# Optimization experiments

Measured on AMD Instinct MI355X. Metric: run time of the kernel, lower is better.

## Reference

```python
import jax, jax.numpy as jnp
import numpy as np

N_NODES = 100000
N_EDGES = 1600000
NODE_DIM = 128
EDGE_DIM = 64
MSG_DIM = 128
NODE_DIM_OUT = 128


def setup_inputs() -> dict:
    key = jax.random.key(0)
    k1, k2, k3, k4, k5, k6, k7 = jax.random.split(key, 7)
    node_emb = jax.random.normal(k1, (N_NODES, NODE_DIM), dtype=jnp.float32)
    edge_index = jax.random.randint(k2, (2, N_EDGES), 0, N_NODES, dtype=jnp.int64)
    edge_emb = jax.random.normal(k3, (N_EDGES, EDGE_DIM), dtype=jnp.float32)
    # Linear params (stored as [in, out]; torch uses [out, in] with x @ W.T)
    s_msg = 1.0 / np.sqrt(NODE_DIM + EDGE_DIM)
    W_msg = jax.random.uniform(k4, (NODE_DIM + EDGE_DIM, MSG_DIM), jnp.float32, -s_msg, s_msg)
    b_msg = jax.random.uniform(k5, (MSG_DIM,), jnp.float32, -s_msg, s_msg)
    s_upd = 1.0 / np.sqrt(NODE_DIM + MSG_DIM)
    W_upd = jax.random.uniform(k6, (NODE_DIM + MSG_DIM, NODE_DIM_OUT), jnp.float32, -s_upd, s_upd)
    b_upd = jax.random.uniform(k7, (NODE_DIM_OUT,), jnp.float32, -s_upd, s_upd)
    return {"node_emb": node_emb, "edge_index": edge_index, "edge_emb": edge_emb,
            "W_msg": W_msg, "b_msg": b_msg, "W_upd": W_upd, "b_upd": b_upd}


def reference(node_emb, edge_index, edge_emb, W_msg, b_msg, W_upd, b_upd):
    # PyG MessagePassing default flow: x_j = x[edge_index[0]] (source),
    # messages aggregated (mean) at edge_index[1] (target).
    src = edge_index[0]
    dst = edge_index[1]
    n = node_emb.shape[0]

    x_j = node_emb[src]                                    # [E, node_dim] gather
    msg_in = jnp.concatenate([x_j, edge_emb], axis=1)      # [E, node_dim+edge_dim]
    msg = jax.nn.relu(msg_in @ W_msg + b_msg)              # [E, msg_dim]

    # scatter-mean aggregate to nodes
    summed = jax.ops.segment_sum(msg, dst, num_segments=n)  # [N, msg_dim]
    counts = jax.ops.segment_sum(jnp.ones((msg.shape[0],), dtype=msg.dtype), dst, num_segments=n)
    mean_msg = summed / jnp.maximum(counts, 1.0)[:, None]

    upd_in = jnp.concatenate([node_emb, mean_msg], axis=1)  # [N, node_dim+msg_dim]
    h = jax.nn.relu(upd_in @ W_upd + b_upd)                 # [N, node_dim_out]
    # dropout is identity in eval mode; normalize=False (default)
    return h
```

## Files before the change

### kernel.cpp

```cpp
#include <hip/hip_runtime.h>
#include <hip/hip_bf16.h>

#define N_NODES 100000
#define N_EDGES 1600000
#define D_NODE 128
#define D_EDGE 64
#define D_MSG 128
#define K1 192
#define K2 256
#define D_OUT 128
#define NSB 98
#define TILE 64
#define NT (N_EDGES / TILE)

using frag8 = __attribute__((ext_vector_type(8))) short;
using facc  = __attribute__((ext_vector_type(4))) float;

static __device__ __forceinline__ unsigned short f2bf(float f) {
    unsigned int u = __float_as_uint(f);
    u = u + 0x7fffu + ((u >> 16) & 1u);
    return (unsigned short)(u >> 16);
}
static __device__ __forceinline__ float bflo(unsigned int u) { return __uint_as_float(u << 16); }
static __device__ __forceinline__ float bfhi(unsigned int u) { return __uint_as_float(u & 0xffff0000u); }

union F8 { unsigned short s[8]; frag8 f; uint4 u4; };

static __device__ __forceinline__ frag8 pack8(float4 a, float4 b) {
    F8 u;
    u.s[0] = f2bf(a.x); u.s[1] = f2bf(a.y); u.s[2] = f2bf(a.z); u.s[3] = f2bf(a.w);
    u.s[4] = f2bf(b.x); u.s[5] = f2bf(b.y); u.s[6] = f2bf(b.z); u.s[7] = f2bf(b.w);
    return u.f;
}

__global__ void prep_all_kernel(const float* __restrict__ Wm, const float* __restrict__ Wu,
                                const float* __restrict__ node_emb, const int* __restrict__ dst,
                                unsigned short* __restrict__ WtM, unsigned short* __restrict__ WtU,
                                unsigned int* __restrict__ nodeB32, int* __restrict__ cnt) {
    int idx0 = blockIdx.x * blockDim.x + threadIdx.x;
    int stride = gridDim.x * blockDim.x;
    for (int idx = idx0; idx < 128 * K1; idx += stride) {
        int o = idx / K1, k = idx - o * K1;
        WtM[idx] = f2bf(Wm[k * D_MSG + o]);
    }
    for (int idx = idx0; idx < 128 * K2; idx += stride) {
        int o = idx >> 8, k = idx & 255;
        WtU[idx] = f2bf(Wu[k * D_OUT + o]);
    }
    const int total = N_NODES * 64;
    for (int i = idx0; i < total; i += stride) {
        float2 v = *(const float2*)&node_emb[(size_t)i * 2];
        nodeB32[i] = (unsigned)f2bf(v.x) | ((unsigned)f2bf(v.y) << 16);
    }
    for (int e = idx0; e < N_EDGES; e += stride) {
        int d = min(max(dst[e], 0), N_NODES - 1);
        atomicAdd(&cnt[d], 1);
    }
}

__global__ __launch_bounds__(1024) void scan_blocks(const int* __restrict__ cnt,
                                                    int* __restrict__ base,
                                                    int* __restrict__ part) {
    __shared__ int sh[1024];
    int i = blockIdx.x * 1024 + threadIdx.x;
    int c = (i < N_NODES) ? cnt[i] : 0;
    sh[threadIdx.x] = c;
    __syncthreads();
    for (int s = 1; s < 1024; s <<= 1) {
        int t = (threadIdx.x >= s) ? sh[threadIdx.x - s] : 0;
        __syncthreads();
        sh[threadIdx.x] += t;
        __syncthreads();
    }
    if (i < N_NODES) base[i] = sh[threadIdx.x] - c;
    if (threadIdx.x == 1023) part[blockIdx.x] = sh[1023];
}

__global__ __launch_bounds__(128) void scan_partials(int* __restrict__ part) {
    __shared__ int sh[128];
    int i = threadIdx.x;
    int c = (i < NSB) ? part[i] : 0;
    sh[i] = c;
    __syncthreads();
    for (int s = 1; s < 128; s <<= 1) {
        int t = (i >= s) ? sh[i - s] : 0;
        __syncthreads();
        sh[i] += t;
        __syncthreads();
    }
    if (i < NSB) part[i] = sh[i] - c;
}

__global__ __launch_bounds__(1024) void scan_add(int* __restrict__ base, const int* __restrict__ part) {
    int i = blockIdx.x * 1024 + threadIdx.x;
    if (i < N_NODES) base[i] += part[blockIdx.x];
}

__global__ void scatter_kernel(const int* __restrict__ dst, const int* __restrict__ src,
                               const int* __restrict__ base, int* __restrict__ cursor,
                               int* __restrict__ perm, int* __restrict__ srcS,
                               int* __restrict__ dstS) {
    int idx0 = blockIdx.x * blockDim.x + threadIdx.x;
    int stride = gridDim.x * blockDim.x;
    for (int e = idx0; e < N_EDGES; e += stride) {
        int d = min(max(dst[e], 0), N_NODES - 1);
        int pos = base[d] + atomicAdd(&cursor[d], 1);
        perm[pos] = e;
        srcS[pos] = src[e];
        dstS[pos] = d;
    }
}

__global__ __launch_bounds__(256, 4) void msg_fused_kernel(
    const unsigned short* __restrict__ nodeB, const int* __restrict__ srcS,
    const int* __restrict__ perm, const int* __restrict__ dstS,
    const float* __restrict__ edge_emb, const unsigned short* __restrict__ WtM,
    const float* __restrict__ b_msg, const int* __restrict__ base,
    const int* __restrict__ cnt, unsigned int* __restrict__ meanB32,
    float* __restrict__ spill)
{
    __shared__ unsigned short sIn[TILE][192];
    __shared__ unsigned short sMsg[TILE][128];

    const int lane = threadIdx.x & 63;
    const int wav  = threadIdx.x >> 6;
    const int j = lane & 15;
    const int q = lane >> 4;

    frag8 wfr[2][6];
#pragma unroll
    for (int m2 = 0; m2 < 2; ++m2) {
        const unsigned short* wrow = WtM + ((wav * 2 + m2) * 16 + j) * K1;
#pragma unroll
        for (int kc = 0; kc < 6; ++kc)
            wfr[m2][kc] = *(const frag8*)&wrow[(kc * 4 + q) * 8];
    }
    float bias[2][4];
#pragma unroll
    for (int m2 = 0; m2 < 2; ++m2)
#pragma unroll
        for (int r = 0; r < 4; ++r) bias[m2][r] = b_msg[(wav * 2 + m2) * 16 + q * 4 + r];

    const int eL = threadIdx.x >> 2;
    const int qt = threadIdx.x & 3;
    const int swz = eL & 7;

    uint4  nst[4];
    float4 est[4];

    const int t0 = blockIdx.x;

    {
        const int e = t0 * TILE + eL;
        const int sp = min(max(srcS[e], 0), N_NODES - 1);
        const unsigned short* nrow = nodeB + (size_t)sp * D_NODE + qt * 32;
#pragma unroll
        for (int i = 0; i < 4; ++i) nst[i] = *(const uint4*)&nrow[i * 8];
        const float* erow = edge_emb + (size_t)perm[e] * D_EDGE + qt * 16;
#pragma unroll
        for (int i = 0; i < 4; ++i) est[i] = *(const float4*)&erow[i * 4];
    }

#pragma unroll 1
    for (int t = t0; t < NT; t += gridDim.x) {
        const int e0 = t * TILE;

        __syncthreads();

        {
            unsigned short* drow = &sIn[eL][0];
#pragma unroll
            for (int i = 0; i < 4; ++i)
                *(uint4*)&drow[((4 * qt + i) ^ swz) * 8] = nst[i];
#pragma unroll
            for (int h = 0; h < 2; ++h) {
                F8 u;
                u.f = pack8(est[h * 2], est[h * 2 + 1]);
                *(uint4*)&drow[((16 + 2 * qt + h) ^ swz) * 8] = u.u4;
            }
        }
        __syncthreads();

        const int tn = t + gridDim.x;
        if (tn < NT) {
            const int e = tn * TILE + eL;
            const int sp = min(max(srcS[e], 0), N_NODES - 1);
            const unsigned short* nrow = nodeB + (size_t)sp * D_NODE + qt * 32;
#pragma unroll
            for (int i = 0; i < 4; ++i) nst[i] = *(const uint4*)&nrow[i * 8];
            const float* erow = edge_emb + (size_t)perm[e] * D_EDGE + qt * 16;
#pragma unroll
            for (int i = 0; i < 4; ++i) est[i] = *(const float4*)&erow[i * 4];
        }

        facc acc[2][4];
#pragma unroll
        for (int m2 = 0; m2 < 2; ++m2)
#pragma unroll
            for (int eg = 0; eg < 4; ++eg) { facc z = {0.f,0.f,0.f,0.f}; acc[m2][eg] = z; }

        const int rsw = j & 7;
#pragma unroll
        for (int eg = 0; eg < 4; ++eg) {
            const unsigned short* irow = &sIn[eg * 16 + j][0];
#pragma unroll
            for (int kc = 0; kc < 6; ++kc) {
                frag8 b = *(const frag8*)&irow[((4 * kc + q) ^ rsw) * 8];
                acc[0][eg] = __builtin_amdgcn_mfma_f32_16x16x32_bf16(wfr[0][kc], b, acc[0][eg], 0, 0, 0);
                acc[1][eg] = __builtin_amdgcn_mfma_f32_16x16x32_bf16(wfr[1][kc], b, acc[1][eg], 0, 0, 0);
            }
        }

#pragma unroll
        for (int eg = 0; eg < 4; ++eg) {
            unsigned short* mrow = &sMsg[eg * 16 + j][0];
#pragma unroll
            for (int m2 = 0; m2 < 2; ++m2) {
                float v0 = fmaxf(acc[m2][eg][0] + bias[m2][0], 0.f);
                float v1 = fmaxf(acc[m2][eg][1] + bias[m2][1], 0.f);
                float v2 = fmaxf(acc[m2][eg][2] + bias[m2][2], 0.f);
                float v3 = fmaxf(acc[m2][eg][3] + bias[m2][3], 0.f);
                uint2 w;
                w.x = (unsigned)f2bf(v0) | ((unsigned)f2bf(v1) << 16);
                w.y = (unsigned)f2bf(v2) | ((unsigned)f2bf(v3) << 16);
                int c64 = wav * 8 + m2 * 4 + q;
                *(uint2*)&mrow[(c64 ^ rsw) * 4] = w;
            }
        }
        __syncthreads();

        const int d_lo = dstS[e0];
        const int d_hi = dstS[e0 + TILE - 1];
        for (int n = d_lo + wav; n <= d_hi; n += 4) {
            const int b = base[n];
            const int c = cnt[n];
            const int lo = max(b - e0, 0);
            const int hi = min(b + c - e0, TILE);
            float s0 = 0.f, s1 = 0.f;
            for (int r = lo; r < hi; ++r) {
                const unsigned* mr = (const unsigned*)&sMsg[r][0];
                unsigned u = mr[(((lane >> 1) ^ (r & 7)) << 1) | (lane & 1)];
                s0 += bflo(u); s1 += bfhi(u);
            }
            const float inv = 1.0f / fmaxf((float)c, 1.0f);
            s0 *= inv; s1 *= inv;
            if (b >= e0 && b + c <= e0 + TILE) {
                meanB32[(size_t)n * 64 + lane] =
                    (unsigned)f2bf(s0) | ((unsigned)f2bf(s1) << 16);
            } else {
                int slot = (n == d_lo) ? 0 : 1;
                *(float2*)(spill + ((size_t)(t * 2 + slot)) * D_MSG + lane * 2) =
                    make_float2(s0, s1);
            }
        }
    }
}

__global__ __launch_bounds__(256) void cleanup_kernel(
    const int* __restrict__ dstS, const int* __restrict__ base,
    const int* __restrict__ cnt, const float* __restrict__ spill,
    unsigned int* __restrict__ meanB32)
{
    const int wav = threadIdx.x >> 6;
    const int lane = threadIdx.x & 63;
    const int n = blockIdx.x * 4 + wav;
    const int c = cnt[n];
    float s0 = 0.f, s1 = 0.f;
    if (c > 0) {
        const int b = base[n];
        const int t0 = b >> 6, t1 = (b + c - 1) >> 6;
        if (t0 == t1) return;
        for (int t = t0; t <= t1; ++t) {
            const int slot = (dstS[t * TILE] == n) ? 0 : 1;
            const float* sp = spill + ((size_t)(t * 2 + slot)) * D_MSG + lane * 2;
            s0 += sp[0]; s1 += sp[1];
        }
    }
    meanB32[(size_t)n * 64 + lane] = (unsigned)f2bf(s0) | ((unsigned)f2bf(s1) << 16);
}

__global__ __launch_bounds__(256) void node_gemm_kernel(
    const unsigned short* __restrict__ nodeB, const unsigned short* __restrict__ meanB,
    const unsigned short* __restrict__ WtU, const float* __restrict__ b_upd,
    float* __restrict__ out)
{
    __shared__ unsigned short sW[128 * K2];

    for (int idx = threadIdx.x; idx < 128 * 32; idx += 256) {
        int o = idx >> 5, ch = idx & 31;
        *(uint4*)&sW[o * K2 + (ch ^ (o & 7)) * 8] = *(const uint4*)&WtU[o * K2 + ch * 8];
    }

    const int lane = threadIdx.x & 63;
    const int wav  = threadIdx.x >> 6;
    const int j = lane & 15;
    const int q = lane >> 4;
    const int rs = j & 7;

    float bias[32];
#pragma unroll
    for (int mt = 0; mt < 8; ++mt)
#pragma unroll
        for (int r = 0; r < 4; ++r) bias[mt * 4 + r] = b_upd[mt * 16 + q * 4 + r];
    __syncthreads();

    const int n0w = blockIdx.x * 256 + wav * 64;

#pragma unroll 1
    for (int g = 0; g < 4; ++g) {
        const int n = n0w + g * 16 + j;
        const bool valid = (n < N_NODES);
        const size_t nn = valid ? (size_t)n : 0;

        frag8 bfr[8];
        const unsigned short* nrow = nodeB + nn * D_NODE;
#pragma unroll
        for (int kc = 0; kc < 4; ++kc)
            bfr[kc] = *(const frag8*)&nrow[kc * 32 + q * 8];
        const unsigned short* mrow = meanB + nn * D_MSG;
#pragma unroll
        for (int kc = 0; kc < 4; ++kc)
            bfr[4 + kc] = *(const frag8*)&mrow[kc * 32 + q * 8];

        facc acc[8];
#pragma unroll
        for (int mt = 0; mt < 8; ++mt) { facc z = {0.f, 0.f, 0.f, 0.f}; acc[mt] = z; }

#pragma unroll
        for (int mt = 0; mt < 8; ++mt) {
            const unsigned short* wrow = &sW[(mt * 16 + j) * K2];
#pragma unroll
            for (int kc = 0; kc < 8; ++kc) {
                frag8 a = *(const frag8*)&wrow[((kc * 4 + q) ^ rs) * 8];
                acc[mt] = __builtin_amdgcn_mfma_f32_16x16x32_bf16(a, bfr[kc], acc[mt], 0, 0, 0);
            }
        }

        if (valid) {
            float* orow = out + (size_t)n * D_OUT;
#pragma unroll
            for (int mt = 0; mt < 8; ++mt)
#pragma unroll
                for (int r = 0; r < 4; ++r)
                    orow[mt * 16 + q * 4 + r] = fmaxf(acc[mt][r] + bias[mt * 4 + r], 0.f);
        }
    }
}

__global__ void prep_w_kernel(const float* __restrict__ Wm, const float* __restrict__ Wu,
                              unsigned short* __restrict__ WtM, unsigned short* __restrict__ WtU) {
    int idx0 = blockIdx.x * blockDim.x + threadIdx.x;
    int stride = gridDim.x * blockDim.x;
    for (int idx = idx0; idx < 128 * K1; idx += stride) {
        int o = idx / K1, k = idx - o * K1;
        WtM[idx] = f2bf(Wm[k * D_MSG + o]);
    }
    for (int idx = idx0; idx < 128 * K2; idx += stride) {
        int o = idx >> 8, k = idx & 255;
        WtU[idx] = f2bf(Wu[k * D_OUT + o]);
    }
}

__global__ void hist_kernel(const int* __restrict__ dst, int* __restrict__ cnt) {
    int idx0 = blockIdx.x * blockDim.x + threadIdx.x;
    int stride = gridDim.x * blockDim.x;
    for (int e = idx0; e < N_EDGES; e += stride) {
        int d = min(max(dst[e], 0), N_NODES - 1);
        atomicAdd(&cnt[d], 1);
    }
}

__global__ __launch_bounds__(256) void msg_agg_kernel_fb(
    const float* __restrict__ node_emb, const int* __restrict__ src,
    const float* __restrict__ edge_emb, const unsigned short* __restrict__ WtM,
    const float* __restrict__ b_msg, const int* __restrict__ perm,
    const int* __restrict__ dstS, const int* __restrict__ cnt,
    float* __restrict__ mean)
{
    __shared__ unsigned short sW[128 * K1];

    for (int idx = threadIdx.x; idx < 128 * 24; idx += 256) {
        int o = idx / 24, ch = idx % 24;
        *(uint4*)&sW[o * K1 + (ch ^ (o & 7)) * 8] = *(const uint4*)&WtM[o * K1 + ch * 8];
    }

    const int lane = threadIdx.x & 63;
    const int wav  = threadIdx.x >> 6;
    const int j = lane & 15;
    const int q = lane >> 4;

    float bias[32];
#pragma unroll
    for (int mt = 0; mt < 8; ++mt)
#pragma unroll
        for (int r = 0; r < 4; ++r) bias[mt * 4 + r] = b_msg[mt * 16 + q * 4 + r];
    __syncthreads();

    const int e0w = blockIdx.x * 256 + wav * 64;
    float carry[32];
    int carry_d = -1;

#pragma unroll 1
    for (int g = 0; g < 4; ++g) {
        const int e = e0w + g * 16 + j;
        const int p = perm[e];
        const int d = dstS[e];
        const int sp = min(max(src[p], 0), N_NODES - 1);
        const float invc = 1.0f / (float)cnt[d];

        frag8 bfr[6];
        const float* nrow = node_emb + (size_t)sp * D_NODE;
#pragma unroll
        for (int kc = 0; kc < 4; ++kc) {
            float4 a = *(const float4*)&nrow[kc * 32 + q * 8];
            float4 c = *(const float4*)&nrow[kc * 32 + q * 8 + 4];
            bfr[kc] = pack8(a, c);
        }
        const float* erow = edge_emb + (size_t)p * D_EDGE;
#pragma unroll
        for (int kc = 0; kc < 2; ++kc) {
            float4 a = *(const float4*)&erow[kc * 32 + q * 8];
            float4 c = *(const float4*)&erow[kc * 32 + q * 8 + 4];
            bfr[4 + kc] = pack8(a, c);
        }

        facc acc[8];
#pragma unroll
        for (int mt = 0; mt < 8; ++mt) { facc z = {0.f, 0.f, 0.f, 0.f}; acc[mt] = z; }

#pragma unroll
        for (int mt = 0; mt < 8; ++mt) {
            const unsigned short* wrow = &sW[(mt * 16 + j) * K1];
            const int rs = j & 7;
#pragma unroll
            for (int kc = 0; kc < 6; ++kc) {
                frag8 a = *(const frag8*)&wrow[((kc * 4 + q) ^ rs) * 8];
                acc[mt] = __builtin_amdgcn_mfma_f32_16x16x32_bf16(a, bfr[kc], acc[mt], 0, 0, 0);
            }
        }

        float v[32];
#pragma unroll
        for (int mt = 0; mt < 8; ++mt)
#pragma unroll
            for (int r = 0; r < 4; ++r) {
                float t = acc[mt][r] + bias[mt * 4 + r];
                v[mt * 4 + r] = fmaxf(t, 0.f) * invc;
            }

        int dprev = __shfl_up(d, 1, 16);
        int head = (j == 0 || d != dprev) ? 1 : 0;
        int seg = head;
#pragma unroll
        for (int s = 1; s < 16; s <<= 1) { int t = __shfl_up(seg, s, 16); if (j >= s) seg += t; }
        int sg1 = __shfl_up(seg, 1, 16);
        int sg2 = __shfl_up(seg, 2, 16);
        int sg4 = __shfl_up(seg, 4, 16);
        int sg8 = __shfl_up(seg, 8, 16);
        bool ok1 = (j >= 1) && (sg1 == seg);
        bool ok2 = (j >= 2) && (sg2 == seg);
        bool ok4 = (j >= 4) && (sg4 == seg);
        bool ok8 = (j >= 8) && (sg8 == seg);

#pragma unroll
        for (int i = 0; i < 32; ++i) { float t = __shfl_up(v[i], 1, 16); if (ok1) v[i] += t; }
#pragma unroll
        for (int i = 0; i < 32; ++i) { float t = __shfl_up(v[i], 2, 16); if (ok2) v[i] += t; }
#pragma unroll
        for (int i = 0; i < 32; ++i) { float t = __shfl_up(v[i], 4, 16); if (ok4) v[i] += t; }
#pragma unroll
        for (int i = 0; i < 32; ++i) { float t = __shfl_up(v[i], 8, 16); if (ok8) v[i] += t; }

        int d0 = __shfl(d, 0, 16);
        if (g > 0) {
            if (d0 != carry_d) {
                if (j == 0) {
                    float* mrow = mean + (size_t)carry_d * D_MSG;
#pragma unroll
                    for (int mt = 0; mt < 8; ++mt)
#pragma unroll
                        for (int r = 0; r < 4; ++r)
                            atomicAdd(&mrow[mt * 16 + q * 4 + r], carry[mt * 4 + r]);
                }
            } else if (seg == 1) {
#pragma unroll
                for (int i = 0; i < 32; ++i) v[i] += carry[i];
            }
        }

#pragma unroll
        for (int i = 0; i < 32; ++i) carry[i] = __shfl(v[i], 15, 16);
        carry_d = __shfl(d, 15, 16);

        int dnext = __shfl_down(d, 1, 16);
        bool tail = (j < 15) ? (dnext != d) : (g == 3);
        if (tail) {
            float* mrow = mean + (size_t)d * D_MSG;
#pragma unroll
            for (int mt = 0; mt < 8; ++mt)
#pragma unroll
                for (int r = 0; r < 4; ++r)
                    atomicAdd(&mrow[mt * 16 + q * 4 + r], v[mt * 4 + r]);
        }
    }
}

__global__ __launch_bounds__(256) void node_kernel_fb(
    const float* __restrict__ node_emb, const float* __restrict__ mean,
    const unsigned short* __restrict__ WtU, const float* __restrict__ b_upd,
    float* __restrict__ out)
{
    __shared__ unsigned short sW[128 * K2];

    for (int idx = threadIdx.x; idx < 128 * 32; idx += 256) {
        int o = idx >> 5, ch = idx & 31;
        *(uint4*)&sW[o * K2 + (ch ^ (o & 7)) * 8] = *(const uint4*)&WtU[o * K2 + ch * 8];
    }

    const int lane = threadIdx.x & 63;
    const int wav  = threadIdx.x >> 6;
    const int j = lane & 15;
    const int q = lane >> 4;

    float bias[32];
#pragma unroll
    for (int mt = 0; mt < 8; ++mt)
#pragma unroll
        for (int r = 0; r < 4; ++r) bias[mt * 4 + r] = b_upd[mt * 16 + q * 4 + r];
    __syncthreads();

    const int n0w = blockIdx.x * 256 + wav * 64;

#pragma unroll 1
    for (int g = 0; g < 4; ++g) {
        const int n = n0w + g * 16 + j;
        const bool valid = (n < N_NODES);
        const size_t nn = valid ? (size_t)n : 0;

        frag8 bfr[8];
        const float* nrow = node_emb + nn * D_NODE;
#pragma unroll
        for (int kc = 0; kc < 4; ++kc) {
            float4 a = *(const float4*)&nrow[kc * 32 + q * 8];
            float4 c = *(const float4*)&nrow[kc * 32 + q * 8 + 4];
            bfr[kc] = pack8(a, c);
        }
        const float* mrow = mean + nn * D_MSG;
#pragma unroll
        for (int kc = 0; kc < 4; ++kc) {
            float4 a = *(const float4*)&mrow[kc * 32 + q * 8];
            float4 c = *(const float4*)&mrow[kc * 32 + q * 8 + 4];
            bfr[4 + kc] = pack8(a, c);
        }

        facc acc[8];
#pragma unroll
        for (int mt = 0; mt < 8; ++mt) { facc z = {0.f, 0.f, 0.f, 0.f}; acc[mt] = z; }

#pragma unroll
        for (int mt = 0; mt < 8; ++mt) {
            const unsigned short* wrow = &sW[(mt * 16 + j) * K2];
            const int rs = j & 7;
#pragma unroll
            for (int kc = 0; kc < 8; ++kc) {
                frag8 a = *(const frag8*)&wrow[((kc * 4 + q) ^ rs) * 8];
                acc[mt] = __builtin_amdgcn_mfma_f32_16x16x32_bf16(a, bfr[kc], acc[mt], 0, 0, 0);
            }
        }

        if (valid) {
            float* orow = out + (size_t)n * D_OUT;
#pragma unroll
            for (int mt = 0; mt < 8; ++mt)
#pragma unroll
                for (int r = 0; r < 4; ++r)
                    orow[mt * 16 + q * 4 + r] = fmaxf(acc[mt][r] + bias[mt * 4 + r], 0.f);
        }
    }
}

extern "C" void kernel_launch(void* const* d_in, const int* in_sizes, int n_in,
                              void* d_out, int out_size, void* d_ws, size_t ws_size,
                              hipStream_t stream) {
    const float* node_emb = (const float*)d_in[0];
    const int*   edge_idx = (const int*)d_in[1];
    const float* edge_emb = (const float*)d_in[2];
    const float* W_msg    = (const float*)d_in[3];
    const float* b_msg    = (const float*)d_in[4];
    const float* W_upd    = (const float*)d_in[5];
    const float* b_upd    = (const float*)d_in[6];
    float* out = (float*)d_out;

    const int* src = edge_idx;
    const int* dst = edge_idx + N_EDGES;

    char* W = (char*)d_ws;

    if (ws_size >= 98000000ULL) {
        unsigned short* meanB = (unsigned short*)(W + 0);
        int* cnt     = (int*)(W + 25600000);
        int* cursor  = (int*)(W + 26000000);
        int* base    = (int*)(W + 26400000);
        int* part    = (int*)(W + 26800000);
        int* perm    = (int*)(W + 26800512);
        int* srcS    = (int*)(W + 33200512);
        int* dstS    = (int*)(W + 39600512);
        unsigned short* WtM   = (unsigned short*)(W + 46000512);
        unsigned short* WtU   = (unsigned short*)(W + 46049664);
        unsigned short* nodeB = (unsigned short*)(W + 46115200);
        float* spill = (float*)(W + 71715200);

        hipMemsetAsync(W + 25600000, 0, 800000, stream);

        prep_all_kernel<<<2048, 256, 0, stream>>>(W_msg, W_upd, node_emb, dst,
                                                  WtM, WtU, (unsigned int*)nodeB, cnt);
        scan_blocks<<<NSB, 1024, 0, stream>>>(cnt, base, part);
        scan_partials<<<1, 128, 0, stream>>>(part);
        scan_add<<<NSB, 1024, 0, stream>>>(base, part);
        scatter_kernel<<<1024, 256, 0, stream>>>(dst, src, base, cursor, perm, srcS, dstS);
        msg_fused_kernel<<<2048, 256, 0, stream>>>(nodeB, srcS, perm, dstS, edge_emb,
                                                   WtM, b_msg, base, cnt,
                                                   (unsigned int*)meanB, spill);
        cleanup_kernel<<<25000, 256, 0, stream>>>(dstS, base, cnt, spill,
                                                  (unsigned int*)meanB);
        node_gemm_kernel<<<391, 256, 0, stream>>>(nodeB, meanB, WtU, b_upd, out);
    } else {
        float* mean  = (float*)W;
        int* cnt     = (int*)(W + 51200000);
        int* cursor  = (int*)(W + 51600000);
        int* base    = (int*)(W + 52000000);
        int* part    = (int*)(W + 52400000);
        int* perm    = (int*)(W + 52400512);
        int* dstS    = (int*)(W + 58800512);
        int* srcS    = (int*)(W + 65200512);
        unsigned short* WtM = (unsigned short*)(W + 71600512);
        unsigned short* WtU = (unsigned short*)(W + 71649664);

        hipMemsetAsync(d_ws, 0, 52000000, stream);

        prep_w_kernel<<<224, 256, 0, stream>>>(W_msg, W_upd, WtM, WtU);
        hist_kernel<<<1024, 256, 0, stream>>>(dst, cnt);
        scan_blocks<<<NSB, 1024, 0, stream>>>(cnt, base, part);
        scan_partials<<<1, 128, 0, stream>>>(part);
        scan_add<<<NSB, 1024, 0, stream>>>(base, part);
        scatter_kernel<<<1024, 256, 0, stream>>>(dst, src, base, cursor, perm, srcS, dstS);
        msg_agg_kernel_fb<<<6250, 256, 0, stream>>>(node_emb, src, edge_emb, WtM,
                                                    b_msg, perm, dstS, cnt, mean);
        node_kernel_fb<<<391, 256, 0, stream>>>(node_emb, mean, WtU, b_upd, out);
    }
}
```

Baseline: 611.1 us.

## Pack sorted edge metadata into one int4 array and use nontemporal memory ops

The scatter kernel now writes edge id, source and destination as a single 16-byte record, replacing three separate arrays. The message kernel reads that one record per edge, and streaming data (edge embeddings, mean outputs, spill) uses nontemporal loads and stores. The separate partial-scan kernel is merged into scan_add, which computes each block's offset with a wave reduction, removing one launch. The message kernel's occupancy hint drops from 4 to 3 blocks. The record wastes one padding word, and the higher workspace threshold could route execution to the fallback path if the workspace is smaller than the new requirement.

```diff
diff --git a/kernel.cpp b/kernel.cpp
--- a/kernel.cpp
+++ b/kernel.cpp
@@ -15,6 +15,9 @@
 
 using frag8 = __attribute__((ext_vector_type(8))) short;
 using facc  = __attribute__((ext_vector_type(4))) float;
+typedef int   i32x4 __attribute__((ext_vector_type(4)));
+typedef float f32x4 __attribute__((ext_vector_type(4)));
+typedef float f32x2 __attribute__((ext_vector_type(2)));
 
 static __device__ __forceinline__ unsigned short f2bf(float f) {
     unsigned int u = __float_as_uint(f);
@@ -30,6 +33,12 @@
     F8 u;
     u.s[0] = f2bf(a.x); u.s[1] = f2bf(a.y); u.s[2] = f2bf(a.z); u.s[3] = f2bf(a.w);
     u.s[4] = f2bf(b.x); u.s[5] = f2bf(b.y); u.s[6] = f2bf(b.z); u.s[7] = f2bf(b.w);
+    return u.f;
+}
+static __device__ __forceinline__ frag8 pack8v(f32x4 a, f32x4 b) {
+    F8 u;
+    u.s[0] = f2bf(a[0]); u.s[1] = f2bf(a[1]); u.s[2] = f2bf(a[2]); u.s[3] = f2bf(a[3]);
+    u.s[4] = f2bf(b[0]); u.s[5] = f2bf(b[1]); u.s[6] = f2bf(b[2]); u.s[7] = f2bf(b[3]);
     return u.f;
 }
 
@@ -76,44 +85,37 @@
     if (threadIdx.x == 1023) part[blockIdx.x] = sh[1023];
 }
 
-__global__ __launch_bounds__(128) void scan_partials(int* __restrict__ part) {
-    __shared__ int sh[128];
-    int i = threadIdx.x;
-    int c = (i < NSB) ? part[i] : 0;
-    sh[i] = c;
+__global__ __launch_bounds__(1024) void scan_add(int* __restrict__ base, const int* __restrict__ part) {
+    __shared__ int soff;
+    if (threadIdx.x < 64) {
+        int l = threadIdx.x;
+        int v = 0;
+        if (l < blockIdx.x) v += part[l];
+        if (l + 64 < blockIdx.x) v += part[l + 64];
+#pragma unroll
+        for (int s = 32; s; s >>= 1) v += __shfl_down(v, s, 64);
+        if (l == 0) soff = v;
+    }
     __syncthreads();
-    for (int s = 1; s < 128; s <<= 1) {
-        int t = (i >= s) ? sh[i - s] : 0;
-        __syncthreads();
-        sh[i] += t;
-        __syncthreads();
-    }
-    if (i < NSB) part[i] = sh[i] - c;
-}
-
-__global__ __launch_bounds__(1024) void scan_add(int* __restrict__ base, const int* __restrict__ part) {
     int i = blockIdx.x * 1024 + threadIdx.x;
-    if (i < N_NODES) base[i] += part[blockIdx.x];
+    if (i < N_NODES) base[i] += soff;
 }
 
 __global__ void scatter_kernel(const int* __restrict__ dst, const int* __restrict__ src,
                                const int* __restrict__ base, int* __restrict__ cursor,
-                               int* __restrict__ perm, int* __restrict__ srcS,
-                               int* __restrict__ dstS) {
+                               i32x4* __restrict__ meta) {
     int idx0 = blockIdx.x * blockDim.x + threadIdx.x;
     int stride = gridDim.x * blockDim.x;
     for (int e = idx0; e < N_EDGES; e += stride) {
         int d = min(max(dst[e], 0), N_NODES - 1);
         int pos = base[d] + atomicAdd(&cursor[d], 1);
-        perm[pos] = e;
-        srcS[pos] = src[e];
-        dstS[pos] = d;
-    }
-}
-
-__global__ __launch_bounds__(256, 4) void msg_fused_kernel(
-    const unsigned short* __restrict__ nodeB, const int* __restrict__ srcS,
-    const int* __restrict__ perm, const int* __restrict__ dstS,
+        i32x4 m; m[0] = e; m[1] = src[e]; m[2] = d; m[3] = 0;
+        __builtin_nontemporal_store(m, &meta[pos]);
+    }
+}
+
+__global__ __launch_bounds__(256, 3) void msg_fused_kernel(
+    const unsigned short* __restrict__ nodeB, const i32x4* __restrict__ meta,
     const float* __restrict__ edge_emb, const unsigned short* __restrict__ WtM,
     const float* __restrict__ b_msg, const int* __restrict__ base,
     const int* __restrict__ cnt, unsigned int* __restrict__ meanB32,
@@ -145,20 +147,22 @@
     const int qt = threadIdx.x & 3;
     const int swz = eL & 7;
 
-    uint4  nst[4];
-    float4 est[4];
+    uint4 nst[4];
+    f32x4 est[4];
 
     const int t0 = blockIdx.x;
 
     {
         const int e = t0 * TILE + eL;
-        const int sp = min(max(srcS[e], 0), N_NODES - 1);
+        const i32x4 m = __builtin_nontemporal_load(&meta[e]);
+        const int sp = min(max(m[1], 0), N_NODES - 1);
         const unsigned short* nrow = nodeB + (size_t)sp * D_NODE + qt * 32;
 #pragma unroll
         for (int i = 0; i < 4; ++i) nst[i] = *(const uint4*)&nrow[i * 8];
-        const float* erow = edge_emb + (size_t)perm[e] * D_EDGE + qt * 16;
-#pragma unroll
-        for (int i = 0; i < 4; ++i) est[i] = *(const float4*)&erow[i * 4];
+        const float* erow = edge_emb + (size_t)m[0] * D_EDGE + qt * 16;
+#pragma unroll
+        for (int i = 0; i < 4; ++i)
+            est[i] = __builtin_nontemporal_load((const f32x4*)&erow[i * 4]);
     }
 
 #pragma unroll 1
@@ -175,7 +179,7 @@
 #pragma unroll
             for (int h = 0; h < 2; ++h) {
                 F8 u;
-                u.f = pack8(est[h * 2], est[h * 2 + 1]);
+                u.f = pack8v(est[h * 2], est[h * 2 + 1]);
                 *(uint4*)&drow[((16 + 2 * qt + h) ^ swz) * 8] = u.u4;
             }
         }
@@ -184,13 +188,15 @@
         const int tn = t + gridDim.x;
         if (tn < NT) {
             const int e = tn * TILE + eL;
-            const int sp = min(max(srcS[e], 0), N_NODES - 1);
+            const i32x4 m = __builtin_nontemporal_load(&meta[e]);
+            const int sp = min(max(m[1], 0), N_NODES - 1);
             const unsigned short* nrow = nodeB + (size_t)sp * D_NODE + qt * 32;
 #pragma unroll
             for (int i = 0; i < 4; ++i) nst[i] = *(const uint4*)&nrow[i * 8];
-            const float* erow = edge_emb + (size_t)perm[e] * D_EDGE + qt * 16;
-#pragma unroll
-            for (int i = 0; i < 4; ++i) est[i] = *(const float4*)&erow[i * 4];
+            const float* erow = edge_emb + (size_t)m[0] * D_EDGE + qt * 16;
+#pragma unroll
+            for (int i = 0; i < 4; ++i)
+                est[i] = __builtin_nontemporal_load((const f32x4*)&erow[i * 4]);
         }
 
         facc acc[2][4];
@@ -229,8 +235,8 @@
         }
         __syncthreads();
 
-        const int d_lo = dstS[e0];
-        const int d_hi = dstS[e0 + TILE - 1];
+        const int d_lo = meta[e0][2];
+        const int d_hi = meta[e0 + TILE - 1][2];
         for (int n = d_lo + wav; n <= d_hi; n += 4) {
             const int b = base[n];
             const int c = cnt[n];
@@ -245,19 +251,20 @@
             const float inv = 1.0f / fmaxf((float)c, 1.0f);
             s0 *= inv; s1 *= inv;
             if (b >= e0 && b + c <= e0 + TILE) {
-                meanB32[(size_t)n * 64 + lane] =
-                    (unsigned)f2bf(s0) | ((unsigned)f2bf(s1) << 16);
+                unsigned int w = (unsigned)f2bf(s0) | ((unsigned)f2bf(s1) << 16);
+                __builtin_nontemporal_store(w, &meanB32[(size_t)n * 64 + lane]);
             } else {
                 int slot = (n == d_lo) ? 0 : 1;
-                *(float2*)(spill + ((size_t)(t * 2 + slot)) * D_MSG + lane * 2) =
-                    make_float2(s0, s1);
+                f32x2 w; w[0] = s0; w[1] = s1;
+                __builtin_nontemporal_store(
+                    w, (f32x2*)(spill + ((size_t)(t * 2 + slot)) * D_MSG + lane * 2));
             }
         }
     }
 }
 
 __global__ __launch_bounds__(256) void cleanup_kernel(
-    const int* __restrict__ dstS, const int* __restrict__ base,
+    const i32x4* __restrict__ meta, const int* __restrict__ base,
     const int* __restrict__ cnt, const float* __restrict__ spill,
     unsigned int* __restrict__ meanB32)
 {
@@ -271,7 +278,7 @@
         const int t0 = b >> 6, t1 = (b + c - 1) >> 6;
         if (t0 == t1) return;
         for (int t = t0; t <= t1; ++t) {
-            const int slot = (dstS[t * TILE] == n) ? 0 : 1;
+            const int slot = (meta[t * TILE][2] == n) ? 0 : 1;
             const float* sp = spill + ((size_t)(t * 2 + slot)) * D_MSG + lane * 2;
             s0 += sp[0]; s1 += sp[1];
         }
@@ -371,10 +378,9 @@
 }
 
 __global__ __launch_bounds__(256) void msg_agg_kernel_fb(
-    const float* __restrict__ node_emb, const int* __restrict__ src,
+    const float* __restrict__ node_emb, const i32x4* __restrict__ meta,
     const float* __restrict__ edge_emb, const unsigned short* __restrict__ WtM,
-    const float* __restrict__ b_msg, const int* __restrict__ perm,
-    const int* __restrict__ dstS, const int* __restrict__ cnt,
+    const float* __restrict__ b_msg, const int* __restrict__ cnt,
     float* __restrict__ mean)
 {
     __shared__ unsigned short sW[128 * K1];
@@ -403,9 +409,10 @@
 #pragma unroll 1
     for (int g = 0; g < 4; ++g) {
         const int e = e0w + g * 16 + j;
-        const int p = perm[e];
-        const int d = dstS[e];
-        const int sp = min(max(src[p], 0), N_NODES - 1);
+        const i32x4 m = meta[e];
+        const int p = m[0];
+        const int d = m[2];
+        const int sp = min(max(m[1], 0), N_NODES - 1);
         const float invc = 1.0f / (float)cnt[d];
 
         frag8 bfr[6];
@@ -596,32 +603,29 @@
 
     char* W = (char*)d_ws;
 
-    if (ws_size >= 98000000ULL) {
+    if (ws_size >= 104000000ULL) {
         unsigned short* meanB = (unsigned short*)(W + 0);
         int* cnt     = (int*)(W + 25600000);
         int* cursor  = (int*)(W + 26000000);
         int* base    = (int*)(W + 26400000);
         int* part    = (int*)(W + 26800000);
-        int* perm    = (int*)(W + 26800512);
-        int* srcS    = (int*)(W + 33200512);
-        int* dstS    = (int*)(W + 39600512);
-        unsigned short* WtM   = (unsigned short*)(W + 46000512);
-        unsigned short* WtU   = (unsigned short*)(W + 46049664);
-        unsigned short* nodeB = (unsigned short*)(W + 46115200);
-        float* spill = (float*)(W + 71715200);
+        i32x4* meta  = (i32x4*)(W + 26800512);
+        unsigned short* WtM   = (unsigned short*)(W + 52400512);
+        unsigned short* WtU   = (unsigned short*)(W + 52449664);
+        unsigned short* nodeB = (unsigned short*)(W + 52515200);
+        float* spill = (float*)(W + 78115200);
 
         hipMemsetAsync(W + 25600000, 0, 800000, stream);
 
         prep_all_kernel<<<2048, 256, 0, stream>>>(W_msg, W_upd, node_emb, dst,
                                                   WtM, WtU, (unsigned int*)nodeB, cnt);
         scan_blocks<<<NSB, 1024, 0, stream>>>(cnt, base, part);
-        scan_partials<<<1, 128, 0, stream>>>(part);
         scan_add<<<NSB, 1024, 0, stream>>>(base, part);
-        scatter_kernel<<<1024, 256, 0, stream>>>(dst, src, base, cursor, perm, srcS, dstS);
-        msg_fused_kernel<<<2048, 256, 0, stream>>>(nodeB, srcS, perm, dstS, edge_emb,
+        scatter_kernel<<<1024, 256, 0, stream>>>(dst, src, base, cursor, meta);
+        msg_fused_kernel<<<2048, 256, 0, stream>>>(nodeB, meta, edge_emb,
                                                    WtM, b_msg, base, cnt,
                                                    (unsigned int*)meanB, spill);
-        cleanup_kernel<<<25000, 256, 0, stream>>>(dstS, base, cnt, spill,
+        cleanup_kernel<<<25000, 256, 0, stream>>>(meta, base, cnt, spill,
                                                   (unsigned int*)meanB);
         node_gemm_kernel<<<391, 256, 0, stream>>>(nodeB, meanB, WtU, b_upd, out);
     } else {
@@ -630,22 +634,19 @@
         int* cursor  = (int*)(W + 51600000);
         int* base    = (int*)(W + 52000000);
         int* part    = (int*)(W + 52400000);
-        int* perm    = (int*)(W + 52400512);
-        int* dstS    = (int*)(W + 58800512);
-        int* srcS    = (int*)(W + 65200512);
-        unsigned short* WtM = (unsigned short*)(W + 71600512);
-        unsigned short* WtU = (unsigned short*)(W + 71649664);
+        i32x4* meta  = (i32x4*)(W + 52400512);
+        unsigned short* WtM = (unsigned short*)(W + 78000512);
+        unsigned short* WtU = (unsigned short*)(W + 78049664);
 
         hipMemsetAsync(d_ws, 0, 52000000, stream);
 
         prep_w_kernel<<<224, 256, 0, stream>>>(W_msg, W_upd, WtM, WtU);
         hist_kernel<<<1024, 256, 0, stream>>>(dst, cnt);
         scan_blocks<<<NSB, 1024, 0, stream>>>(cnt, base, part);
-        scan_partials<<<1, 128, 0, stream>>>(part);
         scan_add<<<NSB, 1024, 0, stream>>>(base, part);
-        scatter_kernel<<<1024, 256, 0, stream>>>(dst, src, base, cursor, perm, srcS, dstS);
-        msg_agg_kernel_fb<<<6250, 256, 0, stream>>>(node_emb, src, edge_emb, WtM,
-                                                    b_msg, perm, dstS, cnt, mean);
+        scatter_kernel<<<1024, 256, 0, stream>>>(dst, src, base, cursor, meta);
+        msg_agg_kernel_fb<<<6250, 256, 0, stream>>>(node_emb, meta, edge_emb, WtM,
+                                                    b_msg, cnt, mean);
         node_kernel_fb<<<391, 256, 0, stream>>>(node_emb, mean, WtU, b_upd, out);
     }
 }
```

After: 620.2 us. No clear change (+1.5%).
